# Optimization experiments

Measured on AMD Instinct MI355X. Metric: run time of the kernel, lower is better.

## Reference

```python
import jax, jax.numpy as jnp
import numpy as np

IN_F = 8192
OUT_F = 8192
R = 16
LORA_ALPHA = 32
BLOCK = 64
SCALING = LORA_ALPHA / R  # 2.0
NUMEL = IN_F * OUT_F


def dequantize_4bit(packed, scales):
    # packed: [numel//2] bytes (stored as int32 in [0,255]); element 2i = low nibble, 2i+1 = high nibble
    low = packed & 0xF
    high = (packed >> 4) & 0xF
    q = jnp.stack([low, high], axis=-1).reshape(-1)          # [numel] ints in [0,15]
    flat = q.astype(jnp.float32) - 8.0                        # signed 4-bit
    flat = (flat.reshape(-1, BLOCK) * scales[:, None]).reshape(-1)  # blockwise scale
    return flat.reshape(OUT_F, IN_F)


def setup_inputs() -> dict:
    key = jax.random.key(0)
    k1, k2, k3, k4, k5 = jax.random.split(key, 5)
    x = jax.random.normal(k1, (1, 64, IN_F), dtype=jnp.float32)
    packed_weights = jax.random.randint(k2, (NUMEL // 2,), 0, 256, dtype=jnp.int32)
    block_scales = jax.random.uniform(k3, (NUMEL // BLOCK,), dtype=jnp.float32) * 0.05
    # kaiming_uniform(a=sqrt(5)) on [R, IN_F] -> bound = 1/sqrt(IN_F)
    bound = 1.0 / np.sqrt(IN_F)
    lora_A = jax.random.uniform(k4, (R, IN_F), minval=-bound, maxval=bound, dtype=jnp.float32)
    # original init is zeros; use small randn for a non-trivial baseline
    lora_B = jax.random.normal(k5, (OUT_F, R), dtype=jnp.float32) * 0.02
    return {"x": x, "packed_weights": packed_weights, "block_scales": block_scales,
            "lora_A": lora_A, "lora_B": lora_B}


def reference(x, packed_weights, block_scales, lora_A, lora_B):
    W = dequantize_4bit(packed_weights, block_scales).astype(x.dtype)  # [OUT_F, IN_F]
    base_out = jnp.einsum('bsi,oi->bso', x, W)                         # no bias (bias_buffer=None)
    lora_out = jnp.einsum('bsr,or->bso', jnp.einsum('bsi,ri->bsr', x, lora_A), lora_B) * SCALING
    return base_out + lora_out
```

## Files before the change

### kernel.cpp

```cpp
#include <hip/hip_runtime.h>
#include <hip/hip_bf16.h>

#define IN_F 8192
#define OUT_F 8192
#define SEQ 64
#define LORA_R 16

typedef __attribute__((ext_vector_type(4))) float f32x4;
typedef __attribute__((ext_vector_type(4))) int i32x4;
typedef __attribute__((ext_vector_type(8))) unsigned short u16x8;
typedef __attribute__((ext_vector_type(4))) unsigned short u16x4;
typedef _Float16 f16x2 __attribute__((ext_vector_type(2)));
typedef _Float16 f16x8 __attribute__((ext_vector_type(8)));

typedef __attribute__((address_space(3))) unsigned int lds_u32;
typedef const __attribute__((address_space(1))) unsigned int glb_u32;

__device__ __forceinline__ void gl_lds16(const void* g, void* l) {
    __builtin_amdgcn_global_load_lds((glb_u32*)g, (lds_u32*)l, 16, 0, 0);
}

__global__ __launch_bounds__(256) void k_prep(
    const float* __restrict__ x, const float* __restrict__ A,
    unsigned short* __restrict__ xb, float* __restrict__ t) {
    __shared__ float part[64];
    const int s = blockIdx.x >> 2, p = blockIdx.x & 3;
    const int w = threadIdx.x >> 6, lane = threadIdx.x & 63;
    const int kbase = p * 2048 + w * 512;
    const float* xr = x + s * IN_F + kbase;

    f32x4 xv[2];
    #pragma unroll
    for (int j = 0; j < 2; ++j) {
        xv[j] = *(const f32x4*)(xr + j * 256 + lane * 4);
        u16x4 h;
        h[0] = __builtin_bit_cast(unsigned short, (_Float16)xv[j].x);
        h[1] = __builtin_bit_cast(unsigned short, (_Float16)xv[j].y);
        h[2] = __builtin_bit_cast(unsigned short, (_Float16)xv[j].z);
        h[3] = __builtin_bit_cast(unsigned short, (_Float16)xv[j].w);
        *(u16x4*)(xb + s * IN_F + kbase + j * 256 + lane * 4) = h;
    }

    float acc[LORA_R];
    #pragma unroll
    for (int r = 0; r < LORA_R; ++r) acc[r] = 0.f;
    #pragma unroll
    for (int r = 0; r < LORA_R; ++r) {
        const float* ar = A + r * IN_F + kbase;
        #pragma unroll
        for (int j = 0; j < 2; ++j) {
            f32x4 av = *(const f32x4*)(ar + j * 256 + lane * 4);
            acc[r] = fmaf(xv[j].x, av.x, acc[r]);
            acc[r] = fmaf(xv[j].y, av.y, acc[r]);
            acc[r] = fmaf(xv[j].z, av.z, acc[r]);
            acc[r] = fmaf(xv[j].w, av.w, acc[r]);
        }
    }
    #pragma unroll
    for (int r = 0; r < LORA_R; ++r) {
        float v = acc[r];
        #pragma unroll
        for (int off = 32; off; off >>= 1) v += __shfl_down(v, off, 64);
        if (lane == 0) part[w * 16 + r] = v;
    }
    __syncthreads();
    if (threadIdx.x < 16)
        t[s * 64 + p * 16 + threadIdx.x] = part[threadIdx.x] + part[16 + threadIdx.x] +
                                           part[32 + threadIdx.x] + part[48 + threadIdx.x];
}

__global__ __launch_bounds__(512, 2) void k_main(
    const int* __restrict__ packed, const float* __restrict__ scales,
    const unsigned short* __restrict__ xb, const float* __restrict__ t,
    const float* __restrict__ B, float* __restrict__ out) {
    __shared__ char lds[115200];
    _Float16* xs = (_Float16*)lds;
    int* wt = (int*)(lds + 65536);
    float* scs = (float*)(lds + 98304);
    float* accs = (float*)lds;
    float* tred = scs;

    const int tid = threadIdx.x;
    const int n0 = blockIdx.x * 32;
    const int w = tid >> 6, lane = tid & 63;
    const int nh = w >> 2, wkk = w & 3;
    const int q = lane >> 4, c16 = lane & 15;

    const int lrow = lane >> 4, lcol = lane & 15;
    const int xr0 = w * 8 + lrow, xr1 = xr0 + 4;
    const int wr  = w * 4 + lrow;
    const unsigned short* xg0 = xb + (size_t)xr0 * IN_F + ((lcol ^ (xr0 & 7)) << 3);
    const unsigned short* xg1 = xb + (size_t)xr1 * IN_F + ((lcol ^ (xr1 & 7)) << 3);
    const int* wgp = packed + (long)(n0 + wr) * (IN_F / 2) + ((lcol ^ (wr & 7)) << 2);

    _Float16* xd0 = xs + w * 8 * 128;
    _Float16* xd1 = xd0 + 4 * 128;
    int* wd = wt + w * 256;

    {
        int row = tid >> 4, g = tid & 15;
        const float* sp = scales + (n0 + row) * (IN_F / 64);
        *(f32x4*)(scs + row * 132 + g * 4)      = *(const f32x4*)(sp + g * 4);
        *(f32x4*)(scs + row * 132 + 64 + g * 4) = *(const f32x4*)(sp + 64 + g * 4);
    }

    f32x4 acc[4];
    #pragma unroll
    for (int mt = 0; mt < 4; ++mt) acc[mt] = (f32x4){0.f, 0.f, 0.f, 0.f};

    const int pvo = (nh * 16 + c16) * 64 + ((wkk * 16 + q * 4) ^ ((c16 & 7) << 2));
    int afo[4];
    #pragma unroll
    for (int mt = 0; mt < 4; ++mt)
        afo[mt] = (mt * 16 + c16) * 128 + ((wkk * 32 + q * 8) ^ ((c16 & 7) << 3));
    const int sco = (nh * 16 + c16) * 132 + (wkk >> 1);

    asm volatile("s_waitcnt lgkmcnt(0)" ::: "memory");
    __builtin_amdgcn_s_barrier();

    #pragma unroll
    for (int c = 0; c < 3; ++c) {
        gl_lds16(xg0 + (size_t)c * 128, xd0 + c * 8192);
        gl_lds16(xg1 + (size_t)c * 128, xd1 + c * 8192);
        gl_lds16(wgp + c * 64,          wd  + c * 2048);
    }

    const f16x2 c1032 = {(_Float16)1032.0f, (_Float16)1032.0f};

    for (int kt = 0; kt < 64; ++kt) {
        if (kt < 62)       asm volatile("s_waitcnt vmcnt(6)" ::: "memory");
        else if (kt == 62) asm volatile("s_waitcnt vmcnt(3)" ::: "memory");
        else               asm volatile("s_waitcnt vmcnt(0)" ::: "memory");
        __builtin_amdgcn_s_barrier();
        __builtin_amdgcn_sched_barrier(0);
        const int cur = kt & 3;
        if (kt < 61) {
            const int nxt = (kt + 3) & 3;
            const size_t xoff = (size_t)(kt + 3) * 128;
            gl_lds16(xg0 + xoff, xd0 + nxt * 8192);
            gl_lds16(xg1 + xoff, xd1 + nxt * 8192);
            gl_lds16(wgp + (kt + 3) * 64, wd + nxt * 2048);
        }
        i32x4 pv = *(const i32x4*)(wt + cur * 2048 + pvo);
        float scf = scs[sco + kt * 2];
        _Float16 sch = (_Float16)scf;
        f16x2 sc2 = {sch, sch};
        f16x8 bf;
        #pragma unroll
        for (int m = 0; m < 4; ++m) {
            unsigned u = ((((unsigned)pv[m] << 12) | (unsigned)pv[m]) & 0x000F000Fu) | 0x64006400u;
            f16x2 h = __builtin_bit_cast(f16x2, u);
            h = (h - c1032) * sc2;
            bf[2 * m] = h.x;
            bf[2 * m + 1] = h.y;
        }
        const _Float16* xbase = xs + cur * 8192;
        #pragma unroll
        for (int mt = 0; mt < 4; ++mt) {
            f16x8 af = *(const f16x8*)(xbase + afo[mt]);
            acc[mt] = __builtin_amdgcn_mfma_f32_16x16x32_f16(af, bf, acc[mt], 0, 0, 0);
        }
    }
    __syncthreads();

    float* myacc = accs + w * (64 * 17);
    #pragma unroll
    for (int mt = 0; mt < 4; ++mt)
        #pragma unroll
        for (int r = 0; r < 4; ++r)
            myacc[(mt * 16 + q * 4 + r) * 17 + c16] = acc[mt][r];
    #pragma unroll
    for (int jj = 0; jj < 2; ++jj) {
        int p2 = tid + jj * 512;
        const float* tp = t + (p2 >> 4) * 64 + (p2 & 15);
        tred[p2] = tp[0] + tp[16] + tp[32] + tp[48];
    }
    __syncthreads();

    #pragma unroll
    for (int j = 0; j < 4; ++j) {
        int p = tid + j * 512;
        int s = p >> 5, c = p & 31;
        const float* ab = accs + (c >> 4) * 4 * (64 * 17) + s * 17 + (c & 15);
        float v = ab[0] + ab[64 * 17] + ab[2 * 64 * 17] + ab[3 * 64 * 17];
        const float* trow = tred + s * 16;
        const float* bp = B + (n0 + c) * LORA_R;
        f32x4 t0 = *(const f32x4*)trow,        t1 = *(const f32x4*)(trow + 4);
        f32x4 t2 = *(const f32x4*)(trow + 8),  t3 = *(const f32x4*)(trow + 12);
        f32x4 b0 = *(const f32x4*)bp,       b1 = *(const f32x4*)(bp + 4);
        f32x4 b2 = *(const f32x4*)(bp + 8), b3 = *(const f32x4*)(bp + 12);
        float lr = t0.x * b0.x + t0.y * b0.y + t0.z * b0.z + t0.w * b0.w
                 + t1.x * b1.x + t1.y * b1.y + t1.z * b1.z + t1.w * b1.w
                 + t2.x * b2.x + t2.y * b2.y + t2.z * b2.z + t2.w * b2.w
                 + t3.x * b3.x + t3.y * b3.y + t3.z * b3.z + t3.w * b3.w;
        v += 2.0f * lr;
        out[s * OUT_F + n0 + c] = v;
    }
}

extern "C" void kernel_launch(void* const* d_in, const int* in_sizes, int n_in,
                              void* d_out, int out_size, void* d_ws, size_t ws_size,
                              hipStream_t stream) {
    const float* x      = (const float*)d_in[0];
    const int* packed   = (const int*)d_in[1];
    const float* scales = (const float*)d_in[2];
    const float* lora_A = (const float*)d_in[3];
    const float* lora_B = (const float*)d_in[4];
    float* out = (float*)d_out;

    unsigned short* xb = (unsigned short*)d_ws;
    float* t = (float*)((char*)d_ws + (size_t)SEQ * IN_F * 2);

    k_prep<<<256, 256, 0, stream>>>(x, lora_A, xb, t);
    k_main<<<256, 512, 0, stream>>>(packed, scales, xb, t, lora_B, out);
}
```

Before: 217.1 us.

## Fuse x conversion and LoRA-A projection into main dequant GEMM kernel

Removes the separate prep kernel. The main kernel now loads fp32 x through registers, converts it to fp16 and writes it into swizzled LDS, pipelined two steps ahead. In the same loop, the first half of the waves compute x·Aᵀ with extra MFMAs, and the result is reduced in LDS for the LoRA epilogue. This saves a kernel launch and the workspace round trip. In exchange, every block redundantly reads fp32 x (twice the bytes of the fp16 copy) and recomputes the LoRA-A product, which adds register pressure and extra work on half the waves.

```diff
diff --git a/kernel.cpp b/kernel.cpp
--- a/kernel.cpp
+++ b/kernel.cpp
@@ -8,8 +8,6 @@
 
 typedef __attribute__((ext_vector_type(4))) float f32x4;
 typedef __attribute__((ext_vector_type(4))) int i32x4;
-typedef __attribute__((ext_vector_type(8))) unsigned short u16x8;
-typedef __attribute__((ext_vector_type(4))) unsigned short u16x4;
 typedef _Float16 f16x2 __attribute__((ext_vector_type(2)));
 typedef _Float16 f16x8 __attribute__((ext_vector_type(8)));
 
@@ -20,58 +18,18 @@
     __builtin_amdgcn_global_load_lds((glb_u32*)g, (lds_u32*)l, 16, 0, 0);
 }
 
-__global__ __launch_bounds__(256) void k_prep(
-    const float* __restrict__ x, const float* __restrict__ A,
-    unsigned short* __restrict__ xb, float* __restrict__ t) {
-    __shared__ float part[64];
-    const int s = blockIdx.x >> 2, p = blockIdx.x & 3;
-    const int w = threadIdx.x >> 6, lane = threadIdx.x & 63;
-    const int kbase = p * 2048 + w * 512;
-    const float* xr = x + s * IN_F + kbase;
-
-    f32x4 xv[2];
-    #pragma unroll
-    for (int j = 0; j < 2; ++j) {
-        xv[j] = *(const f32x4*)(xr + j * 256 + lane * 4);
-        u16x4 h;
-        h[0] = __builtin_bit_cast(unsigned short, (_Float16)xv[j].x);
-        h[1] = __builtin_bit_cast(unsigned short, (_Float16)xv[j].y);
-        h[2] = __builtin_bit_cast(unsigned short, (_Float16)xv[j].z);
-        h[3] = __builtin_bit_cast(unsigned short, (_Float16)xv[j].w);
-        *(u16x4*)(xb + s * IN_F + kbase + j * 256 + lane * 4) = h;
-    }
-
-    float acc[LORA_R];
-    #pragma unroll
-    for (int r = 0; r < LORA_R; ++r) acc[r] = 0.f;
-    #pragma unroll
-    for (int r = 0; r < LORA_R; ++r) {
-        const float* ar = A + r * IN_F + kbase;
-        #pragma unroll
-        for (int j = 0; j < 2; ++j) {
-            f32x4 av = *(const f32x4*)(ar + j * 256 + lane * 4);
-            acc[r] = fmaf(xv[j].x, av.x, acc[r]);
-            acc[r] = fmaf(xv[j].y, av.y, acc[r]);
-            acc[r] = fmaf(xv[j].z, av.z, acc[r]);
-            acc[r] = fmaf(xv[j].w, av.w, acc[r]);
-        }
-    }
-    #pragma unroll
-    for (int r = 0; r < LORA_R; ++r) {
-        float v = acc[r];
-        #pragma unroll
-        for (int off = 32; off; off >>= 1) v += __shfl_down(v, off, 64);
-        if (lane == 0) part[w * 16 + r] = v;
-    }
-    __syncthreads();
-    if (threadIdx.x < 16)
-        t[s * 64 + p * 16 + threadIdx.x] = part[threadIdx.x] + part[16 + threadIdx.x] +
-                                           part[32 + threadIdx.x] + part[48 + threadIdx.x];
-}
-
-__global__ __launch_bounds__(512, 2) void k_main(
-    const int* __restrict__ packed, const float* __restrict__ scales,
-    const unsigned short* __restrict__ xb, const float* __restrict__ t,
+__device__ __forceinline__ f16x8 cvt8(const f32x4 a, const f32x4 b) {
+    f16x8 r;
+    r[0] = (_Float16)a.x; r[1] = (_Float16)a.y; r[2] = (_Float16)a.z; r[3] = (_Float16)a.w;
+    r[4] = (_Float16)b.x; r[5] = (_Float16)b.y; r[6] = (_Float16)b.z; r[7] = (_Float16)b.w;
+    return r;
+}
+
+#define VMCNT(n) asm volatile("s_waitcnt vmcnt(" #n ")" ::: "memory")
+
+__global__ __launch_bounds__(512, 2) void k_fused(
+    const float* __restrict__ x, const int* __restrict__ packed,
+    const float* __restrict__ scales, const float* __restrict__ A,
     const float* __restrict__ B, float* __restrict__ out) {
     __shared__ char lds[115200];
     _Float16* xs = (_Float16*)lds;
@@ -79,23 +37,14 @@
     float* scs = (float*)(lds + 98304);
     float* accs = (float*)lds;
     float* tred = scs;
+    float* tfin = (float*)(lds + 65536);
 
     const int tid = threadIdx.x;
     const int n0 = blockIdx.x * 32;
     const int w = tid >> 6, lane = tid & 63;
     const int nh = w >> 2, wkk = w & 3;
     const int q = lane >> 4, c16 = lane & 15;
-
     const int lrow = lane >> 4, lcol = lane & 15;
-    const int xr0 = w * 8 + lrow, xr1 = xr0 + 4;
-    const int wr  = w * 4 + lrow;
-    const unsigned short* xg0 = xb + (size_t)xr0 * IN_F + ((lcol ^ (xr0 & 7)) << 3);
-    const unsigned short* xg1 = xb + (size_t)xr1 * IN_F + ((lcol ^ (xr1 & 7)) << 3);
-    const int* wgp = packed + (long)(n0 + wr) * (IN_F / 2) + ((lcol ^ (wr & 7)) << 2);
-
-    _Float16* xd0 = xs + w * 8 * 128;
-    _Float16* xd1 = xd0 + 4 * 128;
-    int* wd = wt + w * 256;
 
     {
         int row = tid >> 4, g = tid & 15;
@@ -103,10 +52,19 @@
         *(f32x4*)(scs + row * 132 + g * 4)      = *(const f32x4*)(sp + g * 4);
         *(f32x4*)(scs + row * 132 + 64 + g * 4) = *(const f32x4*)(sp + 64 + g * 4);
     }
-
-    f32x4 acc[4];
-    #pragma unroll
-    for (int mt = 0; mt < 4; ++mt) acc[mt] = (f32x4){0.f, 0.f, 0.f, 0.f};
+    __builtin_amdgcn_sched_barrier(0);
+
+    const int wr = w * 4 + lrow;
+    const int* wgp = packed + (long)(n0 + wr) * (IN_F / 2) + ((lcol ^ (wr & 7)) << 2);
+    int* wd = wt + w * 256;
+
+    const int xr0 = w * 8 + lrow, xr1 = xr0 + 4;
+    const float* xg0 = x + (size_t)xr0 * IN_F + lcol * 8;
+    const float* xg1 = x + (size_t)xr1 * IN_F + lcol * 8;
+    const int xw0 = xr0 * 128 + ((lcol ^ (xr0 & 7)) << 3);
+    const int xw1 = xr1 * 128 + ((lcol ^ (xr1 & 7)) << 3);
+
+    const float* ag = A + (size_t)c16 * IN_F + wkk * 32 + q * 8;
 
     const int pvo = (nh * 16 + c16) * 64 + ((wkk * 16 + q * 4) ^ ((c16 & 7) << 2));
     int afo[4];
@@ -115,31 +73,44 @@
         afo[mt] = (mt * 16 + c16) * 128 + ((wkk * 32 + q * 8) ^ ((c16 & 7) << 3));
     const int sco = (nh * 16 + c16) * 132 + (wkk >> 1);
 
+    f32x4 acc[4], tac[4];
+    #pragma unroll
+    for (int mt = 0; mt < 4; ++mt) {
+        acc[mt] = (f32x4){0.f, 0.f, 0.f, 0.f};
+        tac[mt] = (f32x4){0.f, 0.f, 0.f, 0.f};
+    }
+
+    f32x4 gxA[4], gxB[4], aA[2], aB[2];
+
+    gl_lds16(wgp,       wd);
+    gl_lds16(wgp +  64, wd + 2048);
+    gl_lds16(wgp + 128, wd + 4096);
+    gxA[0] = *(const f32x4*)(xg0);       gxA[1] = *(const f32x4*)(xg0 + 4);
+    gxA[2] = *(const f32x4*)(xg1);       gxA[3] = *(const f32x4*)(xg1 + 4);
+    gxB[0] = *(const f32x4*)(xg0 + 128); gxB[1] = *(const f32x4*)(xg0 + 132);
+    gxB[2] = *(const f32x4*)(xg1 + 128); gxB[3] = *(const f32x4*)(xg1 + 132);
+    if (nh == 0) { aB[0] = *(const f32x4*)(ag); aB[1] = *(const f32x4*)(ag + 4); }
+    *(f16x8*)(xs + xw0) = cvt8(gxA[0], gxA[1]);
+    *(f16x8*)(xs + xw1) = cvt8(gxA[2], gxA[3]);
     asm volatile("s_waitcnt lgkmcnt(0)" ::: "memory");
-    __builtin_amdgcn_s_barrier();
-
-    #pragma unroll
-    for (int c = 0; c < 3; ++c) {
-        gl_lds16(xg0 + (size_t)c * 128, xd0 + c * 8192);
-        gl_lds16(xg1 + (size_t)c * 128, xd1 + c * 8192);
-        gl_lds16(wgp + c * 64,          wd  + c * 2048);
-    }
 
     const f16x2 c1032 = {(_Float16)1032.0f, (_Float16)1032.0f};
 
-    for (int kt = 0; kt < 64; ++kt) {
-        if (kt < 62)       asm volatile("s_waitcnt vmcnt(6)" ::: "memory");
-        else if (kt == 62) asm volatile("s_waitcnt vmcnt(3)" ::: "memory");
-        else               asm volatile("s_waitcnt vmcnt(0)" ::: "memory");
+    auto body = [&](int kt, f32x4 (&gxI)[4], f32x4 (&gxC)[4],
+                    f32x4 (&aI)[2], f32x4 (&aC)[2]) __attribute__((always_inline)) {
         __builtin_amdgcn_s_barrier();
         __builtin_amdgcn_sched_barrier(0);
         const int cur = kt & 3;
-        if (kt < 61) {
-            const int nxt = (kt + 3) & 3;
-            const size_t xoff = (size_t)(kt + 3) * 128;
-            gl_lds16(xg0 + xoff, xd0 + nxt * 8192);
-            gl_lds16(xg1 + xoff, xd1 + nxt * 8192);
-            gl_lds16(wgp + (kt + 3) * 64, wd + nxt * 2048);
+        if (kt <= 60) gl_lds16(wgp + (kt + 3) * 64, wd + ((kt + 3) & 3) * 2048);
+        if (kt <= 61) {
+            const float* p0 = xg0 + (size_t)(kt + 2) * 128;
+            const float* p1 = xg1 + (size_t)(kt + 2) * 128;
+            gxI[0] = *(const f32x4*)(p0); gxI[1] = *(const f32x4*)(p0 + 4);
+            gxI[2] = *(const f32x4*)(p1); gxI[3] = *(const f32x4*)(p1 + 4);
+        }
+        if (nh == 0 && kt <= 62) {
+            const float* pa = ag + (size_t)(kt + 1) * 128;
+            aI[0] = *(const f32x4*)(pa); aI[1] = *(const f32x4*)(pa + 4);
         }
         i32x4 pv = *(const i32x4*)(wt + cur * 2048 + pvo);
         float scf = scs[sco + kt * 2];
@@ -155,11 +126,43 @@
             bf[2 * m + 1] = h.y;
         }
         const _Float16* xbase = xs + cur * 8192;
-        #pragma unroll
-        for (int mt = 0; mt < 4; ++mt) {
-            f16x8 af = *(const f16x8*)(xbase + afo[mt]);
-            acc[mt] = __builtin_amdgcn_mfma_f32_16x16x32_f16(af, bf, acc[mt], 0, 0, 0);
-        }
+        f16x8 af0 = *(const f16x8*)(xbase + afo[0]);
+        f16x8 af1 = *(const f16x8*)(xbase + afo[1]);
+        f16x8 af2 = *(const f16x8*)(xbase + afo[2]);
+        f16x8 af3 = *(const f16x8*)(xbase + afo[3]);
+        acc[0] = __builtin_amdgcn_mfma_f32_16x16x32_f16(af0, bf, acc[0], 0, 0, 0);
+        acc[1] = __builtin_amdgcn_mfma_f32_16x16x32_f16(af1, bf, acc[1], 0, 0, 0);
+        acc[2] = __builtin_amdgcn_mfma_f32_16x16x32_f16(af2, bf, acc[2], 0, 0, 0);
+        acc[3] = __builtin_amdgcn_mfma_f32_16x16x32_f16(af3, bf, acc[3], 0, 0, 0);
+        if (nh == 0) {
+            if (kt <= 60)      VMCNT(7);
+            else if (kt == 61) VMCNT(6);
+            else if (kt == 62) VMCNT(2);
+            else               VMCNT(0);
+        } else {
+            if (kt <= 60)      VMCNT(5);
+            else if (kt == 61) VMCNT(4);
+            else               VMCNT(0);
+        }
+        __builtin_amdgcn_sched_barrier(0);
+        if (nh == 0) {
+            f16x8 afr = cvt8(aC[0], aC[1]);
+            tac[0] = __builtin_amdgcn_mfma_f32_16x16x32_f16(af0, afr, tac[0], 0, 0, 0);
+            tac[1] = __builtin_amdgcn_mfma_f32_16x16x32_f16(af1, afr, tac[1], 0, 0, 0);
+            tac[2] = __builtin_amdgcn_mfma_f32_16x16x32_f16(af2, afr, tac[2], 0, 0, 0);
+            tac[3] = __builtin_amdgcn_mfma_f32_16x16x32_f16(af3, afr, tac[3], 0, 0, 0);
+        }
+        if (kt <= 62) {
+            const int nb = (kt + 1) & 3;
+            *(f16x8*)(xs + nb * 8192 + xw0) = cvt8(gxC[0], gxC[1]);
+            *(f16x8*)(xs + nb * 8192 + xw1) = cvt8(gxC[2], gxC[3]);
+        }
+        asm volatile("s_waitcnt lgkmcnt(0)" ::: "memory");
+    };
+
+    for (int kt = 0; kt < 64; kt += 2) {
+        body(kt,     gxA, gxB, aA, aB);
+        body(kt + 1, gxB, gxA, aB, aA);
     }
     __syncthreads();
 
@@ -169,11 +172,18 @@
         #pragma unroll
         for (int r = 0; r < 4; ++r)
             myacc[(mt * 16 + q * 4 + r) * 17 + c16] = acc[mt][r];
-    #pragma unroll
-    for (int jj = 0; jj < 2; ++jj) {
-        int p2 = tid + jj * 512;
-        const float* tp = t + (p2 >> 4) * 64 + (p2 & 15);
-        tred[p2] = tp[0] + tp[16] + tp[32] + tp[48];
+    if (nh == 0) {
+        #pragma unroll
+        for (int mt = 0; mt < 4; ++mt)
+            #pragma unroll
+            for (int r = 0; r < 4; ++r)
+                tred[w * 1024 + (mt * 16 + q * 4 + r) * 16 + c16] = tac[mt][r];
+    }
+    __syncthreads();
+    {
+        int p = tid;
+        tfin[p]       = tred[p]       + tred[1024 + p]       + tred[2048 + p]       + tred[3072 + p];
+        tfin[p + 512] = tred[p + 512] + tred[1024 + p + 512] + tred[2048 + p + 512] + tred[3072 + p + 512];
     }
     __syncthreads();
 
@@ -183,7 +193,7 @@
         int s = p >> 5, c = p & 31;
         const float* ab = accs + (c >> 4) * 4 * (64 * 17) + s * 17 + (c & 15);
         float v = ab[0] + ab[64 * 17] + ab[2 * 64 * 17] + ab[3 * 64 * 17];
-        const float* trow = tred + s * 16;
+        const float* trow = tfin + s * 16;
         const float* bp = B + (n0 + c) * LORA_R;
         f32x4 t0 = *(const f32x4*)trow,        t1 = *(const f32x4*)(trow + 4);
         f32x4 t2 = *(const f32x4*)(trow + 8),  t3 = *(const f32x4*)(trow + 12);
@@ -208,9 +218,5 @@
     const float* lora_B = (const float*)d_in[4];
     float* out = (float*)d_out;
 
-    unsigned short* xb = (unsigned short*)d_ws;
-    float* t = (float*)((char*)d_ws + (size_t)SEQ * IN_F * 2);
-
-    k_prep<<<256, 256, 0, stream>>>(x, lora_A, xb, t);
-    k_main<<<256, 512, 0, stream>>>(packed, scales, xb, t, lora_B, out);
-}
+    k_fused<<<256, 512, 0, stream>>>(x, packed, scales, lora_A, lora_B, out);
+}
```

Result: slower. 251.9 us (+16.0%).

## Double K-tile width per stage with triple-buffered pipeline and fp16 scales in LDS

Applied to the files above, without the earlier changes.

The main loop now processes a 256-wide K tile per iteration (32 iterations instead of 64), issuing two sets of MFMAs per barrier. The staging buffers drop from four stages of 128 to three stages of 256, and scales are converted to fp16 once when loaded into LDS. The intent is to halve the number of barriers and waitcnts per output tile and to give each wave more independent MFMA work between synchronisation points. In exchange, LDS use grows to about 152 KB per block, which probably limits occupancy to one 512-thread block per CU despite launch_bounds(512,2).

```diff
diff --git a/kernel.cpp b/kernel.cpp
--- a/kernel.cpp
+++ b/kernel.cpp
@@ -8,7 +8,6 @@
 
 typedef __attribute__((ext_vector_type(4))) float f32x4;
 typedef __attribute__((ext_vector_type(4))) int i32x4;
-typedef __attribute__((ext_vector_type(8))) unsigned short u16x8;
 typedef __attribute__((ext_vector_type(4))) unsigned short u16x4;
 typedef _Float16 f16x2 __attribute__((ext_vector_type(2)));
 typedef _Float16 f16x8 __attribute__((ext_vector_type(8)));
@@ -19,6 +18,8 @@
 __device__ __forceinline__ void gl_lds16(const void* g, void* l) {
     __builtin_amdgcn_global_load_lds((glb_u32*)g, (lds_u32*)l, 16, 0, 0);
 }
+
+#define VMCNT(n) asm volatile("s_waitcnt vmcnt(" #n ")" ::: "memory")
 
 __global__ __launch_bounds__(256) void k_prep(
     const float* __restrict__ x, const float* __restrict__ A,
@@ -73,92 +74,121 @@
     const int* __restrict__ packed, const float* __restrict__ scales,
     const unsigned short* __restrict__ xb, const float* __restrict__ t,
     const float* __restrict__ B, float* __restrict__ out) {
-    __shared__ char lds[115200];
+    __shared__ char lds[155904];
     _Float16* xs = (_Float16*)lds;
-    int* wt = (int*)(lds + 65536);
-    float* scs = (float*)(lds + 98304);
+    int* wt = (int*)(lds + 98304);
+    _Float16* scs = (_Float16*)(lds + 147456);
     float* accs = (float*)lds;
-    float* tred = scs;
+    float* tred = (float*)(lds + 36864);
 
     const int tid = threadIdx.x;
     const int n0 = blockIdx.x * 32;
     const int w = tid >> 6, lane = tid & 63;
     const int nh = w >> 2, wkk = w & 3;
     const int q = lane >> 4, c16 = lane & 15;
-
-    const int lrow = lane >> 4, lcol = lane & 15;
-    const int xr0 = w * 8 + lrow, xr1 = xr0 + 4;
-    const int wr  = w * 4 + lrow;
-    const unsigned short* xg0 = xb + (size_t)xr0 * IN_F + ((lcol ^ (xr0 & 7)) << 3);
-    const unsigned short* xg1 = xb + (size_t)xr1 * IN_F + ((lcol ^ (xr1 & 7)) << 3);
-    const int* wgp = packed + (long)(n0 + wr) * (IN_F / 2) + ((lcol ^ (wr & 7)) << 2);
-
-    _Float16* xd0 = xs + w * 8 * 128;
-    _Float16* xd1 = xd0 + 4 * 128;
-    int* wd = wt + w * 256;
+    const int l5 = lane >> 5, l31 = lane & 31;
 
     {
         int row = tid >> 4, g = tid & 15;
         const float* sp = scales + (n0 + row) * (IN_F / 64);
-        *(f32x4*)(scs + row * 132 + g * 4)      = *(const f32x4*)(sp + g * 4);
-        *(f32x4*)(scs + row * 132 + 64 + g * 4) = *(const f32x4*)(sp + 64 + g * 4);
-    }
+        f32x4 a = *(const f32x4*)(sp + g * 4);
+        f32x4 b = *(const f32x4*)(sp + 64 + g * 4);
+        u16x4 ha, hb;
+        ha[0] = __builtin_bit_cast(unsigned short, (_Float16)a.x);
+        ha[1] = __builtin_bit_cast(unsigned short, (_Float16)a.y);
+        ha[2] = __builtin_bit_cast(unsigned short, (_Float16)a.z);
+        ha[3] = __builtin_bit_cast(unsigned short, (_Float16)a.w);
+        hb[0] = __builtin_bit_cast(unsigned short, (_Float16)b.x);
+        hb[1] = __builtin_bit_cast(unsigned short, (_Float16)b.y);
+        hb[2] = __builtin_bit_cast(unsigned short, (_Float16)b.z);
+        hb[3] = __builtin_bit_cast(unsigned short, (_Float16)b.w);
+        *(u16x4*)((unsigned short*)scs + row * 132 + g * 4) = ha;
+        *(u16x4*)((unsigned short*)scs + row * 132 + 64 + g * 4) = hb;
+    }
+
+    const unsigned short* xg[4];
+    #pragma unroll
+    for (int j = 0; j < 4; ++j) {
+        int row = 8 * w + 2 * j + l5;
+        xg[j] = xb + (size_t)row * IN_F + ((l31 ^ (row & 7)) << 3);
+    }
+    _Float16* xd = xs + w * 2048;
+    const int wr0 = 4 * w + l5, wr1 = wr0 + 2;
+    const int* wg0 = packed + (size_t)(n0 + wr0) * (IN_F / 2) + ((l31 ^ (wr0 & 7)) << 2);
+    const int* wg1 = packed + (size_t)(n0 + wr1) * (IN_F / 2) + ((l31 ^ (wr1 & 7)) << 2);
+    int* wd = wt + w * 512;
+
+    const int row_w = nh * 16 + c16, r7 = c16 & 7;
+    const int pvo0 = row_w * 128 + ((4 * wkk + q) ^ r7) * 4;
+    const int pvo1 = row_w * 128 + ((4 * (wkk + 4) + q) ^ r7) * 4;
+    int afo0[4], afo1[4];
+    #pragma unroll
+    for (int mt = 0; mt < 4; ++mt) {
+        afo0[mt] = (mt * 16 + c16) * 256 + ((4 * wkk + q) ^ r7) * 8;
+        afo1[mt] = (mt * 16 + c16) * 256 + ((4 * (wkk + 4) + q) ^ r7) * 8;
+    }
+    const int scso = row_w * 132 + (wkk >> 1);
 
     f32x4 acc[4];
     #pragma unroll
     for (int mt = 0; mt < 4; ++mt) acc[mt] = (f32x4){0.f, 0.f, 0.f, 0.f};
 
-    const int pvo = (nh * 16 + c16) * 64 + ((wkk * 16 + q * 4) ^ ((c16 & 7) << 2));
-    int afo[4];
-    #pragma unroll
-    for (int mt = 0; mt < 4; ++mt)
-        afo[mt] = (mt * 16 + c16) * 128 + ((wkk * 32 + q * 8) ^ ((c16 & 7) << 3));
-    const int sco = (nh * 16 + c16) * 132 + (wkk >> 1);
-
+    #pragma unroll
+    for (int c = 0; c < 2; ++c) {
+        #pragma unroll
+        for (int j = 0; j < 4; ++j)
+            gl_lds16(xg[j] + (size_t)c * 256, xd + c * 16384 + j * 512);
+        gl_lds16(wg0 + (size_t)c * 128, wd + c * 4096);
+        gl_lds16(wg1 + (size_t)c * 128, wd + c * 4096 + 256);
+    }
     asm volatile("s_waitcnt lgkmcnt(0)" ::: "memory");
     __builtin_amdgcn_s_barrier();
 
-    #pragma unroll
-    for (int c = 0; c < 3; ++c) {
-        gl_lds16(xg0 + (size_t)c * 128, xd0 + c * 8192);
-        gl_lds16(xg1 + (size_t)c * 128, xd1 + c * 8192);
-        gl_lds16(wgp + c * 64,          wd  + c * 2048);
-    }
-
     const f16x2 c1032 = {(_Float16)1032.0f, (_Float16)1032.0f};
 
-    for (int kt = 0; kt < 64; ++kt) {
-        if (kt < 62)       asm volatile("s_waitcnt vmcnt(6)" ::: "memory");
-        else if (kt == 62) asm volatile("s_waitcnt vmcnt(3)" ::: "memory");
-        else               asm volatile("s_waitcnt vmcnt(0)" ::: "memory");
+    for (int kt = 0; kt < 32; ++kt) {
+        if (kt < 31) VMCNT(6);
+        else         VMCNT(0);
         __builtin_amdgcn_s_barrier();
         __builtin_amdgcn_sched_barrier(0);
-        const int cur = kt & 3;
-        if (kt < 61) {
-            const int nxt = (kt + 3) & 3;
-            const size_t xoff = (size_t)(kt + 3) * 128;
-            gl_lds16(xg0 + xoff, xd0 + nxt * 8192);
-            gl_lds16(xg1 + xoff, xd1 + nxt * 8192);
-            gl_lds16(wgp + (kt + 3) * 64, wd + nxt * 2048);
-        }
-        i32x4 pv = *(const i32x4*)(wt + cur * 2048 + pvo);
-        float scf = scs[sco + kt * 2];
-        _Float16 sch = (_Float16)scf;
-        f16x2 sc2 = {sch, sch};
-        f16x8 bf;
+        const int cb = kt % 3;
+        if (kt <= 29) {
+            const int nb = (kt + 2) % 3;
+            const size_t xo = (size_t)(kt + 2) * 256;
+            const size_t wo = (size_t)(kt + 2) * 128;
+            #pragma unroll
+            for (int j = 0; j < 4; ++j)
+                gl_lds16(xg[j] + xo, xd + nb * 16384 + j * 512);
+            gl_lds16(wg0 + wo, wd + nb * 4096);
+            gl_lds16(wg1 + wo, wd + nb * 4096 + 256);
+        }
+        i32x4 pv0 = *(const i32x4*)(wt + cb * 4096 + pvo0);
+        i32x4 pv1 = *(const i32x4*)(wt + cb * 4096 + pvo1);
+        _Float16 s0 = scs[scso + kt * 4];
+        _Float16 s1 = scs[scso + kt * 4 + 2];
+        f16x2 sc0 = {s0, s0}, sc1 = {s1, s1};
+        f16x8 bf0, bf1;
         #pragma unroll
         for (int m = 0; m < 4; ++m) {
-            unsigned u = ((((unsigned)pv[m] << 12) | (unsigned)pv[m]) & 0x000F000Fu) | 0x64006400u;
-            f16x2 h = __builtin_bit_cast(f16x2, u);
-            h = (h - c1032) * sc2;
-            bf[2 * m] = h.x;
-            bf[2 * m + 1] = h.y;
-        }
-        const _Float16* xbase = xs + cur * 8192;
+            unsigned u0 = ((((unsigned)pv0[m] << 12) | (unsigned)pv0[m]) & 0x000F000Fu) | 0x64006400u;
+            unsigned u1 = ((((unsigned)pv1[m] << 12) | (unsigned)pv1[m]) & 0x000F000Fu) | 0x64006400u;
+            f16x2 h0 = __builtin_bit_cast(f16x2, u0);
+            f16x2 h1 = __builtin_bit_cast(f16x2, u1);
+            h0 = (h0 - c1032) * sc0;
+            h1 = (h1 - c1032) * sc1;
+            bf0[2 * m] = h0.x; bf0[2 * m + 1] = h0.y;
+            bf1[2 * m] = h1.x; bf1[2 * m + 1] = h1.y;
+        }
+        const _Float16* xbase = xs + cb * 16384;
         #pragma unroll
         for (int mt = 0; mt < 4; ++mt) {
-            f16x8 af = *(const f16x8*)(xbase + afo[mt]);
-            acc[mt] = __builtin_amdgcn_mfma_f32_16x16x32_f16(af, bf, acc[mt], 0, 0, 0);
+            f16x8 af = *(const f16x8*)(xbase + afo0[mt]);
+            acc[mt] = __builtin_amdgcn_mfma_f32_16x16x32_f16(af, bf0, acc[mt], 0, 0, 0);
+        }
+        #pragma unroll
+        for (int mt = 0; mt < 4; ++mt) {
+            f16x8 af = *(const f16x8*)(xbase + afo1[mt]);
+            acc[mt] = __builtin_amdgcn_mfma_f32_16x16x32_f16(af, bf1, acc[mt], 0, 0, 0);
         }
     }
     __syncthreads();
```

Result: faster. 210.3 us (median of 3 runs) (-3.1%).

## Split K across two blocks per tile with separate reduce kernel for LoRA epilogue

Applied to the files above, without the earlier changes.

Splits the K dimension in half so the main kernel launches 512 blocks instead of 256. Each block writes partial sums to a workspace buffer, and a new reduce kernel adds the two halves plus the LoRA term. LDS use drops by going to a 3-stage ring buffer and storing scales as fp16, so launch bounds now allow 4 blocks per CU. The aim is better CU occupancy and memory-level parallelism on the weight stream, at the cost of an extra kernel launch, partial-sum traffic, and a small precision change from converting scales to fp16 before use.

```diff
diff --git a/kernel.cpp b/kernel.cpp
--- a/kernel.cpp
+++ b/kernel.cpp
@@ -8,7 +8,6 @@
 
 typedef __attribute__((ext_vector_type(4))) float f32x4;
 typedef __attribute__((ext_vector_type(4))) int i32x4;
-typedef __attribute__((ext_vector_type(8))) unsigned short u16x8;
 typedef __attribute__((ext_vector_type(4))) unsigned short u16x4;
 typedef _Float16 f16x2 __attribute__((ext_vector_type(2)));
 typedef _Float16 f16x8 __attribute__((ext_vector_type(8)));
@@ -19,6 +18,8 @@
 __device__ __forceinline__ void gl_lds16(const void* g, void* l) {
     __builtin_amdgcn_global_load_lds((glb_u32*)g, (lds_u32*)l, 16, 0, 0);
 }
+
+#define VMCNT(n) asm volatile("s_waitcnt vmcnt(" #n ")" ::: "memory")
 
 __global__ __launch_bounds__(256) void k_prep(
     const float* __restrict__ x, const float* __restrict__ A,
@@ -69,81 +70,84 @@
                                            part[32 + threadIdx.x] + part[48 + threadIdx.x];
 }
 
-__global__ __launch_bounds__(512, 2) void k_main(
+__global__ __launch_bounds__(512, 4) void k_main(
     const int* __restrict__ packed, const float* __restrict__ scales,
-    const unsigned short* __restrict__ xb, const float* __restrict__ t,
-    const float* __restrict__ B, float* __restrict__ out) {
-    __shared__ char lds[115200];
+    const unsigned short* __restrict__ xb, float* __restrict__ pb) {
+    __shared__ char lds[78080];
     _Float16* xs = (_Float16*)lds;
-    int* wt = (int*)(lds + 65536);
-    float* scs = (float*)(lds + 98304);
+    int* wt = (int*)(lds + 49152);
+    _Float16* scs = (_Float16*)(lds + 73728);
     float* accs = (float*)lds;
-    float* tred = scs;
 
     const int tid = threadIdx.x;
-    const int n0 = blockIdx.x * 32;
+    const int tile = blockIdx.x >> 1, kh = blockIdx.x & 1;
+    const int n0 = tile * 32;
     const int w = tid >> 6, lane = tid & 63;
     const int nh = w >> 2, wkk = w & 3;
     const int q = lane >> 4, c16 = lane & 15;
-
-    const int lrow = lane >> 4, lcol = lane & 15;
-    const int xr0 = w * 8 + lrow, xr1 = xr0 + 4;
-    const int wr  = w * 4 + lrow;
-    const unsigned short* xg0 = xb + (size_t)xr0 * IN_F + ((lcol ^ (xr0 & 7)) << 3);
-    const unsigned short* xg1 = xb + (size_t)xr1 * IN_F + ((lcol ^ (xr1 & 7)) << 3);
-    const int* wgp = packed + (long)(n0 + wr) * (IN_F / 2) + ((lcol ^ (wr & 7)) << 2);
-
-    _Float16* xd0 = xs + w * 8 * 128;
-    _Float16* xd1 = xd0 + 4 * 128;
-    int* wd = wt + w * 256;
+    const int lr4 = lane >> 4, slot = lane & 15;
 
     {
         int row = tid >> 4, g = tid & 15;
-        const float* sp = scales + (n0 + row) * (IN_F / 64);
-        *(f32x4*)(scs + row * 132 + g * 4)      = *(const f32x4*)(sp + g * 4);
-        *(f32x4*)(scs + row * 132 + 64 + g * 4) = *(const f32x4*)(sp + 64 + g * 4);
-    }
+        f32x4 a = *(const f32x4*)(scales + (n0 + row) * (IN_F / 64) + kh * 64 + g * 4);
+        u16x4 ha;
+        ha[0] = __builtin_bit_cast(unsigned short, (_Float16)a.x);
+        ha[1] = __builtin_bit_cast(unsigned short, (_Float16)a.y);
+        ha[2] = __builtin_bit_cast(unsigned short, (_Float16)a.z);
+        ha[3] = __builtin_bit_cast(unsigned short, (_Float16)a.w);
+        *(u16x4*)((unsigned short*)scs + row * 68 + g * 4) = ha;
+    }
+
+    const unsigned short* xg[2];
+    #pragma unroll
+    for (int j = 0; j < 2; ++j) {
+        int row = 8 * w + 4 * j + lr4;
+        xg[j] = xb + (size_t)row * IN_F + kh * 4096 + ((slot ^ (row & 7)) << 3);
+    }
+    _Float16* xd0 = xs + (8 * w) * 128;
+    const int wrow = 4 * w + lr4;
+    const int* wg = packed + (size_t)(n0 + wrow) * (IN_F / 2) + kh * 2048 + ((slot ^ (wrow & 7)) << 2);
+    int* wd = wt + (4 * w) * 64;
+
+    const int r7 = c16 & 7;
+    const int ks = (4 * wkk + q) ^ r7;
+    const int pvo = (nh * 16 + c16) * 64 + (ks << 2);
+    int afo[4];
+    #pragma unroll
+    for (int mt = 0; mt < 4; ++mt)
+        afo[mt] = (mt * 16 + c16) * 128 + (ks << 3);
+    const int scso = (nh * 16 + c16) * 68 + (wkk >> 1);
 
     f32x4 acc[4];
     #pragma unroll
     for (int mt = 0; mt < 4; ++mt) acc[mt] = (f32x4){0.f, 0.f, 0.f, 0.f};
 
-    const int pvo = (nh * 16 + c16) * 64 + ((wkk * 16 + q * 4) ^ ((c16 & 7) << 2));
-    int afo[4];
-    #pragma unroll
-    for (int mt = 0; mt < 4; ++mt)
-        afo[mt] = (mt * 16 + c16) * 128 + ((wkk * 32 + q * 8) ^ ((c16 & 7) << 3));
-    const int sco = (nh * 16 + c16) * 132 + (wkk >> 1);
-
+    #pragma unroll
+    for (int c = 0; c < 2; ++c) {
+        gl_lds16(xg[0] + (size_t)c * 128, xd0 + c * 8192);
+        gl_lds16(xg[1] + (size_t)c * 128, xd0 + c * 8192 + 512);
+        gl_lds16(wg + (size_t)c * 64, wd + c * 2048);
+    }
     asm volatile("s_waitcnt lgkmcnt(0)" ::: "memory");
     __builtin_amdgcn_s_barrier();
 
-    #pragma unroll
-    for (int c = 0; c < 3; ++c) {
-        gl_lds16(xg0 + (size_t)c * 128, xd0 + c * 8192);
-        gl_lds16(xg1 + (size_t)c * 128, xd1 + c * 8192);
-        gl_lds16(wgp + c * 64,          wd  + c * 2048);
-    }
-
     const f16x2 c1032 = {(_Float16)1032.0f, (_Float16)1032.0f};
 
-    for (int kt = 0; kt < 64; ++kt) {
-        if (kt < 62)       asm volatile("s_waitcnt vmcnt(6)" ::: "memory");
-        else if (kt == 62) asm volatile("s_waitcnt vmcnt(3)" ::: "memory");
-        else               asm volatile("s_waitcnt vmcnt(0)" ::: "memory");
+    for (int kt = 0; kt < 32; ++kt) {
+        if (kt < 31) VMCNT(3);
+        else         VMCNT(0);
         __builtin_amdgcn_s_barrier();
         __builtin_amdgcn_sched_barrier(0);
-        const int cur = kt & 3;
-        if (kt < 61) {
-            const int nxt = (kt + 3) & 3;
-            const size_t xoff = (size_t)(kt + 3) * 128;
-            gl_lds16(xg0 + xoff, xd0 + nxt * 8192);
-            gl_lds16(xg1 + xoff, xd1 + nxt * 8192);
-            gl_lds16(wgp + (kt + 3) * 64, wd + nxt * 2048);
-        }
-        i32x4 pv = *(const i32x4*)(wt + cur * 2048 + pvo);
-        float scf = scs[sco + kt * 2];
-        _Float16 sch = (_Float16)scf;
+        const int cb = kt % 3;
+        if (kt <= 29) {
+            const int nb = (kt + 2) % 3;
+            const size_t xo = (size_t)(kt + 2) * 128;
+            gl_lds16(xg[0] + xo, xd0 + nb * 8192);
+            gl_lds16(xg[1] + xo, xd0 + nb * 8192 + 512);
+            gl_lds16(wg + (size_t)(kt + 2) * 64, wd + nb * 2048);
+        }
+        i32x4 pv = *(const i32x4*)(wt + cb * 2048 + pvo);
+        _Float16 sch = scs[scso + kt * 2];
         f16x2 sc2 = {sch, sch};
         f16x8 bf;
         #pragma unroll
@@ -154,7 +158,7 @@
             bf[2 * m] = h.x;
             bf[2 * m + 1] = h.y;
         }
-        const _Float16* xbase = xs + cur * 8192;
+        const _Float16* xbase = xs + cb * 8192;
         #pragma unroll
         for (int mt = 0; mt < 4; ++mt) {
             f16x8 af = *(const f16x8*)(xbase + afo[mt]);
@@ -169,33 +173,61 @@
         #pragma unroll
         for (int r = 0; r < 4; ++r)
             myacc[(mt * 16 + q * 4 + r) * 17 + c16] = acc[mt][r];
+    __syncthreads();
+
+    {
+        const int base = tid * 4;
+        f32x4 v4;
+        #pragma unroll
+        for (int j = 0; j < 4; ++j) {
+            int p = base + j;
+            int s = p >> 5, c = p & 31;
+            const float* ab = accs + (c >> 4) * 4 * (64 * 17) + s * 17 + (c & 15);
+            v4[j] = ab[0] + ab[64 * 17] + ab[2 * 64 * 17] + ab[3 * 64 * 17];
+        }
+        *(f32x4*)(pb + ((size_t)(kh * 256 + tile)) * 2048 + base) = v4;
+    }
+}
+
+__global__ __launch_bounds__(512) void k_reduce(
+    const float* __restrict__ pb, const float* __restrict__ t,
+    const float* __restrict__ B, float* __restrict__ out) {
+    __shared__ float tred[64 * 17];
+    __shared__ float bs[32 * 17];
+    const int tid = threadIdx.x;
+    const int tile = blockIdx.x, n0 = tile * 32;
+
     #pragma unroll
     for (int jj = 0; jj < 2; ++jj) {
         int p2 = tid + jj * 512;
-        const float* tp = t + (p2 >> 4) * 64 + (p2 & 15);
-        tred[p2] = tp[0] + tp[16] + tp[32] + tp[48];
-    }
-    __syncthreads();
-
+        int s = p2 >> 4, r = p2 & 15;
+        const float* tp = t + s * 64 + r;
+        tred[s * 17 + r] = tp[0] + tp[16] + tp[32] + tp[48];
+    }
+    {
+        int row = tid >> 4, r = tid & 15;
+        bs[row * 17 + r] = B[(size_t)(n0 + row) * LORA_R + r];
+    }
+    __syncthreads();
+
+    const int base = tid * 4;
+    const float* p0 = pb + (size_t)tile * 2048 + base;
+    const float* p1 = pb + (size_t)(256 + tile) * 2048 + base;
+    f32x4 a = *(const f32x4*)p0;
+    f32x4 b = *(const f32x4*)p1;
+    f32x4 v4;
+    const int s = base >> 5;
+    const float* trow = tred + s * 17;
     #pragma unroll
     for (int j = 0; j < 4; ++j) {
-        int p = tid + j * 512;
-        int s = p >> 5, c = p & 31;
-        const float* ab = accs + (c >> 4) * 4 * (64 * 17) + s * 17 + (c & 15);
-        float v = ab[0] + ab[64 * 17] + ab[2 * 64 * 17] + ab[3 * 64 * 17];
-        const float* trow = tred + s * 16;
-        const float* bp = B + (n0 + c) * LORA_R;
-        f32x4 t0 = *(const f32x4*)trow,        t1 = *(const f32x4*)(trow + 4);
-        f32x4 t2 = *(const f32x4*)(trow + 8),  t3 = *(const f32x4*)(trow + 12);
-        f32x4 b0 = *(const f32x4*)bp,       b1 = *(const f32x4*)(bp + 4);
-        f32x4 b2 = *(const f32x4*)(bp + 8), b3 = *(const f32x4*)(bp + 12);
-        float lr = t0.x * b0.x + t0.y * b0.y + t0.z * b0.z + t0.w * b0.w
-                 + t1.x * b1.x + t1.y * b1.y + t1.z * b1.z + t1.w * b1.w
-                 + t2.x * b2.x + t2.y * b2.y + t2.z * b2.z + t2.w * b2.w
-                 + t3.x * b3.x + t3.y * b3.y + t3.z * b3.z + t3.w * b3.w;
-        v += 2.0f * lr;
-        out[s * OUT_F + n0 + c] = v;
-    }
+        int c = (base + j) & 31;
+        const float* brow = bs + c * 17;
+        float lr = 0.f;
+        #pragma unroll
+        for (int r = 0; r < 16; ++r) lr = fmaf(trow[r], brow[r], lr);
+        v4[j] = a[j] + b[j] + 2.0f * lr;
+    }
+    *(f32x4*)(out + (size_t)s * OUT_F + n0 + (base & 31)) = v4;
 }
 
 extern "C" void kernel_launch(void* const* d_in, const int* in_sizes, int n_in,
@@ -209,8 +241,10 @@
     float* out = (float*)d_out;
 
     unsigned short* xb = (unsigned short*)d_ws;
-    float* t = (float*)((char*)d_ws + (size_t)SEQ * IN_F * 2);
+    float* t  = (float*)((char*)d_ws + (size_t)SEQ * IN_F * 2);
+    float* pb = (float*)((char*)d_ws + 2 * 1024 * 1024);
 
     k_prep<<<256, 256, 0, stream>>>(x, lora_A, xb, t);
-    k_main<<<256, 512, 0, stream>>>(packed, scales, xb, t, lora_B, out);
-}
+    k_main<<<512, 512, 0, stream>>>(packed, scales, xb, pb);
+    k_reduce<<<256, 512, 0, stream>>>(pb, t, lora_B, out);
+}
```

Result: no change. 215.3 us (-0.8%).
